# Kernel tuning notes

Measured on AMD Instinct MI355X. Metric: run time of the kernel, lower is better.

Reference implementation:

```python
import jax, jax.numpy as jnp
import numpy as np

B, S, V = 1, 4096, 50265
D, H, DH, FF, L = 768, 12, 64, 3072, 12
W = 256  # one-sided window (longformer-base attention_window=512)
EPS = 1e-5
NEG = -1e9


def _ln(x, s, b):
    mu = jnp.mean(x, -1, keepdims=True)
    var = jnp.mean(jnp.square(x - mu), -1, keepdims=True)
    return (x - mu) * jax.lax.rsqrt(var + EPS) * s + b


def _sliding_attn(q, k, v, key_mask):
    # q,k,v: [B,H,S,DH]; key_mask: [B,S] (1 = attend). Banded attention |i-j| <= W.
    b, h, s, dh = q.shape
    c = W
    nc = s // c
    idx = jnp.arange(nc)[:, None] * c + jnp.arange(3 * c)[None, :]  # index into padded key axis
    kp = jnp.pad(k, ((0, 0), (0, 0), (c, c), (0, 0)))
    vp = jnp.pad(v, ((0, 0), (0, 0), (c, c), (0, 0)))
    k3 = kp[:, :, idx]  # [B,H,nc,3c,DH]
    v3 = vp[:, :, idx]
    qc = q.reshape(b, h, nc, c, dh)
    scores = jnp.einsum('bhncd,bhnmd->bhncm', qc, k3) * (1.0 / (dh ** 0.5))
    rel = jnp.arange(3 * c)[None, :] - c - jnp.arange(c)[:, None]  # key_pos - query_pos, [c,3c]
    band = jnp.abs(rel) <= W
    km = jnp.pad(key_mask.astype(bool), ((0, 0), (c, c)))[:, idx]  # [B,nc,3c]
    valid = band[None, None, None] & km[:, None, :, None, :]
    probs = jax.nn.softmax(jnp.where(valid, scores, NEG), axis=-1)
    out = jnp.einsum('bhncm,bhnmd->bhncd', probs, v3)
    return out.reshape(b, h, s, dh)


def _forward(input_ids, attention_mask, word_emb, pos_emb, emb_ln_s, emb_ln_b,
             Wq, bq, Wk, bk, Wv, bv, Wo, bo, ln1_s, ln1_b,
             W1, b1, W2, b2, ln2_s, ln2_b,
             h1w, h1b, h2w, h2b, h3w, h3b):
    b, s = input_ids.shape
    pos = jnp.arange(s) + 2  # roberta-style position offset (padding_idx=1)
    x = word_emb[input_ids] + pos_emb[pos][None]
    x = _ln(x, emb_ln_s, emb_ln_b)
    key_mask = attention_mask

    def block(xc, p):
        wq, bq_, wk, bk_, wv, bv_, wo, bo_, l1s, l1b, w1, b1_, w2, b2_, l2s, l2b = p
        q = (xc @ wq + bq_).reshape(b, s, H, DH).transpose(0, 2, 1, 3)
        k = (xc @ wk + bk_).reshape(b, s, H, DH).transpose(0, 2, 1, 3)
        v = (xc @ wv + bv_).reshape(b, s, H, DH).transpose(0, 2, 1, 3)
        a = _sliding_attn(q, k, v, key_mask).transpose(0, 2, 1, 3).reshape(b, s, D)
        xc = _ln(xc + a @ wo + bo_, l1s, l1b)
        hdd = jax.nn.gelu(xc @ w1 + b1_, approximate=False)
        xc = _ln(xc + hdd @ w2 + b2_, l2s, l2b)
        return xc, None

    x, _ = jax.lax.scan(block, x, (Wq, bq, Wk, bk, Wv, bv, Wo, bo,
                                   ln1_s, ln1_b, W1, b1, W2, b2, ln2_s, ln2_b))

    # gather hidden state at last occurrence of token id 2 (</s>) per row
    eq = (input_ids == 2).astype(jnp.int32)
    sep = s - 1 - jnp.argmax(eq[:, ::-1], axis=1)
    emb = x[jnp.arange(b), sep]  # [B, D]

    z = jax.nn.relu(emb @ h1w + h1b)
    z = jax.nn.relu(z @ h2w + h2b)
    return jnp.tanh(z @ h3w + h3b)  # [B, 1]


def setup_inputs() -> dict:
    key = jax.random.key(0)
    ks = jax.random.split(key, 24)
    sc = 0.02

    def n(k, shape):
        return jax.random.normal(k, shape, jnp.float32) * sc

    input_ids = jax.random.randint(ks[0], (B, S), 0, V)
    input_ids = input_ids.at[:, -1].set(2)  # guarantee a </s> token (id 2)
    attention_mask = jnp.ones((B, S), jnp.int32)
    return {
        'input_ids': input_ids,
        'attention_mask': attention_mask,
        'word_emb': n(ks[1], (V, D)),
        'pos_emb': n(ks[2], (S + 2, D)),
        'emb_ln_s': jnp.ones((D,), jnp.float32),
        'emb_ln_b': jnp.zeros((D,), jnp.float32),
        'Wq': n(ks[3], (L, D, D)), 'bq': jnp.zeros((L, D), jnp.float32),
        'Wk': n(ks[4], (L, D, D)), 'bk': jnp.zeros((L, D), jnp.float32),
        'Wv': n(ks[5], (L, D, D)), 'bv': jnp.zeros((L, D), jnp.float32),
        'Wo': n(ks[6], (L, D, D)), 'bo': jnp.zeros((L, D), jnp.float32),
        'ln1_s': jnp.ones((L, D), jnp.float32), 'ln1_b': jnp.zeros((L, D), jnp.float32),
        'W1': n(ks[7], (L, D, FF)), 'b1': jnp.zeros((L, FF), jnp.float32),
        'W2': n(ks[8], (L, FF, D)), 'b2': jnp.zeros((L, D), jnp.float32),
        'ln2_s': jnp.ones((L, D), jnp.float32), 'ln2_b': jnp.zeros((L, D), jnp.float32),
        'h1w': n(ks[9], (D, 512)), 'h1b': jnp.zeros((512,), jnp.float32),
        'h2w': n(ks[10], (512, 256)), 'h2b': jnp.zeros((256,), jnp.float32),
        'h3w': n(ks[11], (256, 1)), 'h3b': jnp.zeros((1,), jnp.float32),
    }


def reference(input_ids, attention_mask, word_emb, pos_emb, emb_ln_s, emb_ln_b,
              Wq, bq, Wk, bk, Wv, bv, Wo, bo, ln1_s, ln1_b,
              W1, b1, W2, b2, ln2_s, ln2_b,
              h1w, h1b, h2w, h2b, h3w, h3b):
    return _forward(input_ids, attention_mask, word_emb, pos_emb, emb_ln_s, emb_ln_b,
                    Wq, bq, Wk, bk, Wv, bv, Wo, bo, ln1_s, ln1_b,
                    W1, b1, W2, b2, ln2_s, ln2_b,
                    h1w, h1b, h2w, h2b, h3w, h3b)
```

## Files before the change

kernel.cpp:

```cpp
#include <hip/hip_runtime.h>
#include <math.h>

#define S_LEN 4096
#define DMODEL 768
#define NHEAD 12
#define DHEAD 64
#define FFDIM 3072
#define NLAYER 12
#define WIN 256
#define QKVN 2304

typedef __bf16 bf16x8 __attribute__((ext_vector_type(8)));
typedef unsigned short u16x8 __attribute__((ext_vector_type(8)));
typedef float f32x4 __attribute__((ext_vector_type(4)));

__device__ inline unsigned short f2bf(float f) {
    unsigned int u = __float_as_uint(f);
    u += 0x7fff + ((u >> 16) & 1);
    return (unsigned short)(u >> 16);
}

__device__ inline void gload16(const void* g, void* l) {
    __builtin_amdgcn_global_load_lds((const __attribute__((address_space(1))) void*)g,
                                     (__attribute__((address_space(3))) void*)l, 16, 0, 0);
}


__device__ inline void block_reduce2(float& sum, float& sq) {
    #pragma unroll
    for (int off = 32; off; off >>= 1) {
        sum += __shfl_xor(sum, off);
        sq  += __shfl_xor(sq, off);
    }
    __shared__ float red[8];
    int wid = threadIdx.x >> 6, lane = threadIdx.x & 63;
    if (lane == 0) { red[wid] = sum; red[wid + 4] = sq; }
    __syncthreads();
    sum = red[0] + red[1] + red[2] + red[3];
    sq  = red[4] + red[5] + red[6] + red[7];
    __syncthreads();
}

__global__ __launch_bounds__(256) void ln_kernel(const float* __restrict__ in,
                                                 const float* __restrict__ s,
                                                 const float* __restrict__ b,
                                                 float* __restrict__ out,
                                                 unsigned short* __restrict__ outb) {
    int row = blockIdx.x, tid = threadIdx.x;
    const float* p = in + (size_t)row * DMODEL;
    float v0 = p[tid], v1 = p[tid + 256], v2 = p[tid + 512];
    float sum = v0 + v1 + v2;
    float sq  = v0 * v0 + v1 * v1 + v2 * v2;
    block_reduce2(sum, sq);
    float mu = sum * (1.0f / DMODEL);
    float var = sq * (1.0f / DMODEL) - mu * mu;
    float rs = rsqrtf(var + 1e-5f);
    float* o = out + (size_t)row * DMODEL;
    unsigned short* ob = outb + (size_t)row * DMODEL;
    float r0 = (v0 - mu) * rs * s[tid]       + b[tid];
    float r1 = (v1 - mu) * rs * s[tid + 256] + b[tid + 256];
    float r2 = (v2 - mu) * rs * s[tid + 512] + b[tid + 512];
    o[tid] = r0; o[tid + 256] = r1; o[tid + 512] = r2;
    ob[tid] = f2bf(r0); ob[tid + 256] = f2bf(r1); ob[tid + 512] = f2bf(r2);
}

__global__ __launch_bounds__(256) void embed_ln_kernel(const int* __restrict__ ids,
                                                       const float* __restrict__ wemb,
                                                       const float* __restrict__ pemb,
                                                       const float* __restrict__ s,
                                                       const float* __restrict__ b,
                                                       float* __restrict__ out,
                                                       unsigned short* __restrict__ outb) {
    int row = blockIdx.x, tid = threadIdx.x;
    int id = ids[row];
    const float* wp = wemb + (size_t)id * DMODEL;
    const float* pp = pemb + (size_t)(row + 2) * DMODEL;
    float v0 = wp[tid] + pp[tid];
    float v1 = wp[tid + 256] + pp[tid + 256];
    float v2 = wp[tid + 512] + pp[tid + 512];
    float sum = v0 + v1 + v2;
    float sq  = v0 * v0 + v1 * v1 + v2 * v2;
    block_reduce2(sum, sq);
    float mu = sum * (1.0f / DMODEL);
    float var = sq * (1.0f / DMODEL) - mu * mu;
    float rs = rsqrtf(var + 1e-5f);
    float* o = out + (size_t)row * DMODEL;
    unsigned short* ob = outb + (size_t)row * DMODEL;
    float r0 = (v0 - mu) * rs * s[tid]       + b[tid];
    float r1 = (v1 - mu) * rs * s[tid + 256] + b[tid + 256];
    float r2 = (v2 - mu) * rs * s[tid + 512] + b[tid + 512];
    o[tid] = r0; o[tid + 256] = r1; o[tid + 512] = r2;
    ob[tid] = f2bf(r0); ob[tid + 256] = f2bf(r1); ob[tid + 512] = f2bf(r2);
}

__global__ __launch_bounds__(256) void transpose_all(const float* __restrict__ wq,
                                                     const float* __restrict__ wk,
                                                     const float* __restrict__ wv,
                                                     const float* __restrict__ wo,
                                                     const float* __restrict__ w1,
                                                     const float* __restrict__ w2,
                                                     unsigned short* __restrict__ dq,
                                                     unsigned short* __restrict__ dk,
                                                     unsigned short* __restrict__ dv,
                                                     unsigned short* __restrict__ dwo,
                                                     unsigned short* __restrict__ d1,
                                                     unsigned short* __restrict__ d2) {
    const int id = blockIdx.x;
    const float* src; unsigned short* dst; int C, R, bx, by;
    if (id < 2304) {
        const int m = id / 576, t2 = id % 576;
        src = (m == 0) ? wq : (m == 1) ? wk : (m == 2) ? wv : wo;
        dst = (m == 0) ? dq : (m == 1) ? dk : (m == 2) ? dv : dwo;
        R = 768; C = 768; bx = (t2 % 24) * 32; by = (t2 / 24) * 32;
    } else if (id < 4608) {
        const int t2 = id - 2304;
        src = w1; dst = d1; R = 768; C = 3072;
        bx = (t2 % 96) * 32; by = (t2 / 96) * 32;
    } else {
        const int t2 = id - 4608;
        src = w2; dst = d2; R = 3072; C = 768;
        bx = (t2 % 24) * 32; by = (t2 / 24) * 32;
    }
    __shared__ float tile[32][33];
    const int t = threadIdx.x;
    const int lrow = t >> 3;
    const int lcol = (t & 7) * 4;
    float4 v = *(const float4*)&src[(size_t)(by + lrow) * C + bx + lcol];
    tile[lrow][lcol]     = v.x;
    tile[lrow][lcol + 1] = v.y;
    tile[lrow][lcol + 2] = v.z;
    tile[lrow][lcol + 3] = v.w;
    __syncthreads();
    const int c  = t >> 3;
    const int rp = t & 7;
    unsigned int b0 = f2bf(tile[4 * rp][c]);
    unsigned int b1 = f2bf(tile[4 * rp + 1][c]);
    unsigned int b2 = f2bf(tile[4 * rp + 2][c]);
    unsigned int b3 = f2bf(tile[4 * rp + 3][c]);
    uint2 pk;
    pk.x = (b1 << 16) | b0;
    pk.y = (b3 << 16) | b2;
    *(uint2*)&dst[(size_t)(bx + c) * R + by + 4 * rp] = pk;
}

__global__ __launch_bounds__(256) void bias_concat(const float* __restrict__ bq,
                                                   const float* __restrict__ bk,
                                                   const float* __restrict__ bv,
                                                   float* __restrict__ out) {
    int l = blockIdx.x, t = threadIdx.x;
    for (int i = t; i < DMODEL; i += 256) {
        out[(size_t)l * QKVN + i]              = bq[(size_t)l * DMODEL + i];
        out[(size_t)l * QKVN + DMODEL + i]     = bk[(size_t)l * DMODEL + i];
        out[(size_t)l * QKVN + 2 * DMODEL + i] = bv[(size_t)l * DMODEL + i];
    }
}

template<int MODE, int BN>
__global__ __launch_bounds__(256) void mfma_gemm(const unsigned short* __restrict__ A,
                                                 const unsigned short* __restrict__ Bt,
                                                 const float* __restrict__ bias,
                                                 const float* __restrict__ res,
                                                 void* __restrict__ Cout,
                                                 int M, int N, int K) {
    constexpr int MR = (BN == 128) ? 4 : 2;
    __shared__ unsigned short As[128 * 64];
    __shared__ unsigned short Bs[BN * 64];
    const int tid = threadIdx.x;
    const int wv = tid >> 6, lane = tid & 63;
    const int bm = blockIdx.x * 128, bn = blockIdx.y * BN;
    const int wr = (BN == 128) ? (wv >> 1) * 64 : wv * 32;
    const int wc = (BN == 128) ? (wv & 1) * 64 : 0;
    const int l15 = lane & 15, g = lane >> 4;

    f32x4 acc[MR][4];
    #pragma unroll
    for (int m = 0; m < MR; ++m)
        #pragma unroll
        for (int n = 0; n < 4; ++n)
            #pragma unroll
            for (int e = 0; e < 4; ++e) acc[m][n][e] = 0.f;

    const int srow = tid >> 3;
    const int scol = (tid & 7) * 8;

    for (int k0 = 0; k0 < K; k0 += 64) {
        __syncthreads();
        #pragma unroll
        for (int c = 0; c < 4; ++c)
            gload16(A + (size_t)(bm + c * 32 + srow) * K + k0 + scol,
                    (char*)As + c * 4096 + wv * 1024);
        #pragma unroll
        for (int c = 0; c < BN / 32; ++c)
            gload16(Bt + (size_t)(bn + c * 32 + srow) * K + k0 + scol,
                    (char*)Bs + c * 4096 + wv * 1024);
        __syncthreads();
        #pragma unroll
        for (int kk = 0; kk < 2; ++kk) {
            bf16x8 af[MR], bfr[4];
            #pragma unroll
            for (int m = 0; m < MR; ++m)
                af[m] = *(const bf16x8*)(As + (wr + m * 16 + l15) * 64 + kk * 32 + g * 8);
            #pragma unroll
            for (int n = 0; n < 4; ++n)
                bfr[n] = *(const bf16x8*)(Bs + (wc + n * 16 + l15) * 64 + kk * 32 + g * 8);
            #pragma unroll
            for (int m = 0; m < MR; ++m)
                #pragma unroll
                for (int n = 0; n < 4; ++n)
                    acc[m][n] = __builtin_amdgcn_mfma_f32_16x16x32_bf16(af[m], bfr[n], acc[m][n], 0, 0, 0);
        }
    }

    #pragma unroll
    for (int m = 0; m < MR; ++m) {
        const int row0 = bm + wr + m * 16 + g * 4;
        #pragma unroll
        for (int n = 0; n < 4; ++n) {
            const int col = bn + wc + n * 16 + l15;
            const float bb = bias[col];
            #pragma unroll
            for (int r = 0; r < 4; ++r) {
                float v = acc[m][n][r] + bb;
                if (MODE == 0) {
                    v += res[(size_t)(row0 + r) * N + col];
                    ((float*)Cout)[(size_t)(row0 + r) * N + col] = v;
                } else if (MODE == 1) {
                    ((unsigned short*)Cout)[(size_t)(row0 + r) * N + col] = f2bf(v);
                } else {
                    float gv = 0.5f * v * (1.0f + erff(v * 0.70710678118654752f));
                    ((unsigned short*)Cout)[(size_t)(row0 + r) * N + col] = f2bf(gv);
                }
            }
        }
    }
}

__global__ __launch_bounds__(256) void attn_mfma(const unsigned short* __restrict__ qkv,
                                                 const int* __restrict__ msk,
                                                 unsigned short* __restrict__ aout) {
    __shared__ unsigned short Ks[2][64 * 64];
    __shared__ unsigned short Vt[2][64 * 64];
    __shared__ unsigned short Ps[4][16 * 64];
    const int tid = threadIdx.x;
    const int wv = tid >> 6, lane = tid & 63;
    const int l15 = lane & 15, g = lane >> 4;
    const int h = blockIdx.y;
    const int q0 = blockIdx.x * 64;

    const int qrow = q0 + wv * 16 + l15;
    bf16x8 qf[2];
    #pragma unroll
    for (int kk = 0; kk < 2; ++kk)
        qf[kk] = *(const bf16x8*)(qkv + (size_t)qrow * QKVN + h * 64 + kk * 32 + g * 8);

    f32x4 o[4];
    #pragma unroll
    for (int n = 0; n < 4; ++n)
        #pragma unroll
        for (int e = 0; e < 4; ++e) o[n][e] = 0.f;
    float mst[4] = {-3e38f, -3e38f, -3e38f, -3e38f};
    float lst[4] = {0.f, 0.f, 0.f, 0.f};

    const int srow = tid >> 3;
    const int scol = (tid & 7) * 8;
    const int xr  = (l15 & 7) << 3;
    const int xb  = (scol >> 3) & 7;

    {
        const int kc = q0 - 256;
        #pragma unroll
        for (int cc = 0; cc < 2; ++cc) {
            const int r = cc * 32 + srow;
            int krow = min(max(kc + r, 0), S_LEN - 1);
            gload16(qkv + (size_t)krow * QKVN + DMODEL + h * 64 + (scol ^ ((r & 7) << 3)),
                    (char*)Ks[0] + cc * 4096 + wv * 1024);
        }
        #pragma unroll
        for (int cc = 0; cc < 2; ++cc) {
            const int r = cc * 32 + srow;
            int vrow = min(max(kc + r, 0), S_LEN - 1);
            u16x8 vvv = *(const u16x8*)(qkv + (size_t)vrow * QKVN + 2 * DMODEL + h * 64 + scol);
            #pragma unroll
            for (int j = 0; j < 8; ++j)
                Vt[0][(scol + j) * 64 + (r ^ ((xb ^ j) << 3))] = vvv[j];
        }
        __syncthreads();
    }

    for (int c = 0; c < 9; ++c) {
        const int cur = c & 1, nxt = cur ^ 1;
        const int kc = q0 - 256 + c * 64;

        if (c < 8) {
            const int kcn = kc + 64;
            #pragma unroll
            for (int cc = 0; cc < 2; ++cc) {
                const int r = cc * 32 + srow;
                int krow = min(max(kcn + r, 0), S_LEN - 1);
                gload16(qkv + (size_t)krow * QKVN + DMODEL + h * 64 + (scol ^ ((r & 7) << 3)),
                        (char*)Ks[nxt] + cc * 4096 + wv * 1024);
            }
            #pragma unroll
            for (int cc = 0; cc < 2; ++cc) {
                const int r = cc * 32 + srow;
                int vrow = min(max(kcn + r, 0), S_LEN - 1);
                u16x8 vvv = *(const u16x8*)(qkv + (size_t)vrow * QKVN + 2 * DMODEL + h * 64 + scol);
                #pragma unroll
                for (int j = 0; j < 8; ++j)
                    Vt[nxt][(scol + j) * 64 + (r ^ ((xb ^ j) << 3))] = vvv[j];
            }
        }

        f32x4 s[4];
        #pragma unroll
        for (int n = 0; n < 4; ++n)
            #pragma unroll
            for (int e = 0; e < 4; ++e) s[n][e] = 0.f;
        #pragma unroll
        for (int kk = 0; kk < 2; ++kk) {
            #pragma unroll
            for (int n = 0; n < 4; ++n) {
                bf16x8 kf = *(const bf16x8*)(Ks[cur] + (n * 16 + l15) * 64 + ((kk * 32 + g * 8) ^ xr));
                s[n] = __builtin_amdgcn_mfma_f32_16x16x32_bf16(qf[kk], kf, s[n], 0, 0, 0);
            }
        }

        float pv[4][4];
        const int qbase = q0 + wv * 16 + g * 4;
        #pragma unroll
        for (int n = 0; n < 4; ++n) {
            const int key = kc + n * 16 + l15;
            const bool kin = (key >= 0) && (key < S_LEN);
            const int mv = kin ? msk[key] : 0;
            #pragma unroll
            for (int r = 0; r < 4; ++r) {
                const int qa = qbase + r;
                const bool valid = (mv != 0) && (abs(key - qa) <= WIN);
                pv[n][r] = valid ? s[n][r] * 0.125f : -1e9f;
            }
        }
        float scold[4];
        #pragma unroll
        for (int r = 0; r < 4; ++r) {
            float mx = fmaxf(fmaxf(pv[0][r], pv[1][r]), fmaxf(pv[2][r], pv[3][r]));
            mx = fmaxf(mx, __shfl_xor(mx, 1));
            mx = fmaxf(mx, __shfl_xor(mx, 2));
            mx = fmaxf(mx, __shfl_xor(mx, 4));
            mx = fmaxf(mx, __shfl_xor(mx, 8));
            const float nm = fmaxf(mst[r], mx);
            scold[r] = expf(mst[r] - nm);
            float sum = 0.f;
            #pragma unroll
            for (int n = 0; n < 4; ++n) { pv[n][r] = expf(pv[n][r] - nm); sum += pv[n][r]; }
            sum += __shfl_xor(sum, 1); sum += __shfl_xor(sum, 2);
            sum += __shfl_xor(sum, 4); sum += __shfl_xor(sum, 8);
            lst[r] = lst[r] * scold[r] + sum;
            mst[r] = nm;
        }
        #pragma unroll
        for (int n = 0; n < 4; ++n)
            #pragma unroll
            for (int r = 0; r < 4; ++r)
                o[n][r] *= scold[r];

        #pragma unroll
        for (int n = 0; n < 4; ++n)
            #pragma unroll
            for (int r = 0; r < 4; ++r) {
                const int ql = g * 4 + r;
                Ps[wv][ql * 64 + ((n * 16 + l15) ^ ((ql & 7) << 3))] = f2bf(pv[n][r]);
            }

        #pragma unroll
        for (int kk = 0; kk < 2; ++kk) {
            bf16x8 pf = *(const bf16x8*)(Ps[wv] + l15 * 64 + ((kk * 32 + g * 8) ^ xr));
            #pragma unroll
            for (int nd = 0; nd < 4; ++nd) {
                const int d = nd * 16 + l15;
                const int xv = (((nd * 2 + (l15 >> 3)) & 7) ^ (l15 & 7)) << 3;
                bf16x8 vf = *(const bf16x8*)(Vt[cur] + d * 64 + ((kk * 32 + g * 8) ^ xv));
                o[nd] = __builtin_amdgcn_mfma_f32_16x16x32_bf16(pf, vf, o[nd], 0, 0, 0);
            }
        }

        __syncthreads();
    }

    #pragma unroll
    for (int r = 0; r < 4; ++r) {
        const float inv = 1.0f / lst[r];
        const int qa = q0 + wv * 16 + g * 4 + r;
        #pragma unroll
        for (int nd = 0; nd < 4; ++nd)
            aout[(size_t)qa * DMODEL + h * 64 + nd * 16 + l15] = f2bf(o[nd][r] * inv);
    }
}

__global__ __launch_bounds__(256) void head1_kernel(const int* __restrict__ ids,
                                                    const float* __restrict__ x,
                                                    const float* __restrict__ w1,
                                                    const float* __restrict__ b1,
                                                    float* __restrict__ z1) {
    const int tid = threadIdx.x;
    __shared__ int sred[256];
    int loc = -1;
    for (int i = tid; i < S_LEN; i += 256)
        if (ids[i] == 2) loc = i;
    sred[tid] = loc;
    __syncthreads();
    for (int s2 = 128; s2; s2 >>= 1) {
        if (tid < s2) sred[tid] = max(sred[tid], sred[tid + s2]);
        __syncthreads();
    }
    const int sep = sred[0] < 0 ? (S_LEN - 1) : sred[0];

    __shared__ float emb[DMODEL];
    for (int d = tid; d < DMODEL; d += 256) emb[d] = x[(size_t)sep * DMODEL + d];
    __syncthreads();

    const int o = blockIdx.x * 64 + (tid & 63);
    const int chunk = tid >> 6;
    float s = 0.f;
    const int d0 = chunk * 192;
    for (int d = d0; d < d0 + 192; ++d)
        s += emb[d] * w1[(size_t)d * 512 + o];
    __shared__ float part[4][64];
    part[chunk][tid & 63] = s;
    __syncthreads();
    if (chunk == 0) {
        float v = part[0][tid] + part[1][tid] + part[2][tid] + part[3][tid] + b1[o];
        z1[o] = fmaxf(v, 0.f);
    }
}

__global__ __launch_bounds__(256) void head2_kernel(const float* __restrict__ z1,
                                                    const float* __restrict__ w2,
                                                    const float* __restrict__ b2,
                                                    const float* __restrict__ w3,
                                                    const float* __restrict__ b3,
                                                    float* __restrict__ out) {
    const int tid = threadIdx.x;
    __shared__ float z1s[512];
    for (int i = tid; i < 512; i += 256) z1s[i] = z1[i];
    __syncthreads();
    float s = b2[tid];
    for (int d = 0; d < 512; ++d) s += z1s[d] * w2[(size_t)d * 256 + tid];
    float z2 = fmaxf(s, 0.f);
    __shared__ float fred[256];
    fred[tid] = z2 * w3[tid];
    __syncthreads();
    for (int s2 = 128; s2; s2 >>= 1) {
        if (tid < s2) fred[tid] += fred[tid + s2];
        __syncthreads();
    }
    if (tid == 0) out[0] = tanhf(fred[0] + b3[0]);
}


extern "C" void kernel_launch(void* const* d_in, const int* in_sizes, int n_in,
                              void* d_out, int out_size, void* d_ws, size_t ws_size,
                              hipStream_t stream) {
    const int*   ids      = (const int*)d_in[0];
    const int*   amask    = (const int*)d_in[1];
    const float* word_emb = (const float*)d_in[2];
    const float* pos_emb  = (const float*)d_in[3];
    const float* emb_s    = (const float*)d_in[4];
    const float* emb_b    = (const float*)d_in[5];
    const float* Wq = (const float*)d_in[6];
    const float* bq = (const float*)d_in[7];
    const float* Wk = (const float*)d_in[8];
    const float* bk = (const float*)d_in[9];
    const float* Wv = (const float*)d_in[10];
    const float* bv = (const float*)d_in[11];
    const float* Wo = (const float*)d_in[12];
    const float* bo = (const float*)d_in[13];
    const float* l1s = (const float*)d_in[14];
    const float* l1b = (const float*)d_in[15];
    const float* W1 = (const float*)d_in[16];
    const float* b1 = (const float*)d_in[17];
    const float* W2 = (const float*)d_in[18];
    const float* b2 = (const float*)d_in[19];
    const float* l2s = (const float*)d_in[20];
    const float* l2b = (const float*)d_in[21];
    const float* h1w = (const float*)d_in[22];
    const float* h1b = (const float*)d_in[23];
    const float* h2w = (const float*)d_in[24];
    const float* h2b = (const float*)d_in[25];
    const float* h3w = (const float*)d_in[26];
    const float* h3b = (const float*)d_in[27];

    char* ws = (char*)d_ws;
    float* x          = (float*)(ws);
    float* t          = (float*)(ws + 12582912);
    unsigned short* xb   = (unsigned short*)(ws + 25165824);
    unsigned short* qkv  = (unsigned short*)(ws + 31457280);
    unsigned short* a    = (unsigned short*)(ws + 50331648);
    unsigned short* hb   = (unsigned short*)(ws + 56623104);
    unsigned short* WqkvT= (unsigned short*)(ws + 81788928);
    unsigned short* WoT  = (unsigned short*)(ws + 85327872);
    unsigned short* W1T  = (unsigned short*)(ws + 86507520);
    unsigned short* W2T  = (unsigned short*)(ws + 91226112);
    float* biascat       = (float*)(ws + 95944704);
    float* z1ws          = (float*)(ws + 96055296);

    bias_concat<<<NLAYER, 256, 0, stream>>>(bq, bk, bv, biascat);
    embed_ln_kernel<<<S_LEN, 256, 0, stream>>>(ids, word_emb, pos_emb, emb_s, emb_b, x, xb);

    const size_t dd = (size_t)DMODEL * DMODEL;
    const size_t df = (size_t)DMODEL * FFDIM;

    for (int l = 0; l < NLAYER; ++l) {
        transpose_all<<<6912, 256, 0, stream>>>(Wq + l * dd, Wk + l * dd, Wv + l * dd, Wo + l * dd,
                                                W1 + l * df, W2 + l * df,
                                                WqkvT, WqkvT + dd, WqkvT + 2 * dd, WoT, W1T, W2T);

        mfma_gemm<1, 128><<<dim3(32, 18), 256, 0, stream>>>(xb, WqkvT, biascat + (size_t)l * QKVN,
                                                            nullptr, qkv, S_LEN, QKVN, DMODEL);
        attn_mfma<<<dim3(S_LEN / 64, NHEAD), 256, 0, stream>>>(qkv, amask, a);

        mfma_gemm<0, 64><<<dim3(32, 12), 256, 0, stream>>>(a, WoT, bo + (size_t)l * DMODEL,
                                                           x, t, S_LEN, DMODEL, DMODEL);
        ln_kernel<<<S_LEN, 256, 0, stream>>>(t, l1s + (size_t)l * DMODEL, l1b + (size_t)l * DMODEL, x, xb);

        mfma_gemm<2, 128><<<dim3(32, 24), 256, 0, stream>>>(xb, W1T, b1 + (size_t)l * FFDIM,
                                                            nullptr, hb, S_LEN, FFDIM, DMODEL);
        mfma_gemm<0, 64><<<dim3(32, 12), 256, 0, stream>>>(hb, W2T, b2 + (size_t)l * DMODEL,
                                                           x, t, S_LEN, DMODEL, FFDIM);
        ln_kernel<<<S_LEN, 256, 0, stream>>>(t, l2s + (size_t)l * DMODEL, l2b + (size_t)l * DMODEL, x, xb);
    }

    head1_kernel<<<8, 256, 0, stream>>>(ids, x, h1w, h1b, z1ws);
    head2_kernel<<<1, 256, 0, stream>>>(z1ws, h2w, h2b, h3w, h3b, (float*)d_out);
}
```

Baseline: 2.774 ms.

## Use one wave per row in LayerNorm and single-buffer attention K/V with vectorized V transpose

The LayerNorm kernel now handles four rows per block, one wavefront per row, with float4 loads and stores and a pure shuffle reduction, so the shared-memory reduction and block barriers go away. The attention kernel drops K/V double buffering in favour of a single LDS buffer loaded each chunk. The V transpose now gathers 4x4 tiles with 8-byte loads and writes 4-element vectors into LDS instead of scalar 16-bit stores. This lowers LDS use and store instruction count, but loses the overlap of the next chunk's loads with the current chunk's MFMA work.

```diff
diff --git a/kernel.cpp b/kernel.cpp
--- a/kernel.cpp
+++ b/kernel.cpp
@@ -12,6 +12,7 @@
 
 typedef __bf16 bf16x8 __attribute__((ext_vector_type(8)));
 typedef unsigned short u16x8 __attribute__((ext_vector_type(8)));
+typedef unsigned short u16x4 __attribute__((ext_vector_type(4)));
 typedef float f32x4 __attribute__((ext_vector_type(4)));
 
 __device__ inline unsigned short f2bf(float f) {
@@ -23,22 +24,6 @@
 __device__ inline void gload16(const void* g, void* l) {
     __builtin_amdgcn_global_load_lds((const __attribute__((address_space(1))) void*)g,
                                      (__attribute__((address_space(3))) void*)l, 16, 0, 0);
-}
-
-
-__device__ inline void block_reduce2(float& sum, float& sq) {
-    #pragma unroll
-    for (int off = 32; off; off >>= 1) {
-        sum += __shfl_xor(sum, off);
-        sq  += __shfl_xor(sq, off);
-    }
-    __shared__ float red[8];
-    int wid = threadIdx.x >> 6, lane = threadIdx.x & 63;
-    if (lane == 0) { red[wid] = sum; red[wid + 4] = sq; }
-    __syncthreads();
-    sum = red[0] + red[1] + red[2] + red[3];
-    sq  = red[4] + red[5] + red[6] + red[7];
-    __syncthreads();
 }
 
 __global__ __launch_bounds__(256) void ln_kernel(const float* __restrict__ in,
@@ -46,22 +31,59 @@
                                                  const float* __restrict__ b,
                                                  float* __restrict__ out,
                                                  unsigned short* __restrict__ outb) {
-    int row = blockIdx.x, tid = threadIdx.x;
+    const int wv = threadIdx.x >> 6, lane = threadIdx.x & 63;
+    const int row = blockIdx.x * 4 + wv;
     const float* p = in + (size_t)row * DMODEL;
-    float v0 = p[tid], v1 = p[tid + 256], v2 = p[tid + 512];
-    float sum = v0 + v1 + v2;
-    float sq  = v0 * v0 + v1 * v1 + v2 * v2;
-    block_reduce2(sum, sq);
-    float mu = sum * (1.0f / DMODEL);
-    float var = sq * (1.0f / DMODEL) - mu * mu;
-    float rs = rsqrtf(var + 1e-5f);
+    const int c = lane * 4;
+    float4 v0 = *(const float4*)&p[c];
+    float4 v1 = *(const float4*)&p[c + 256];
+    float4 v2 = *(const float4*)&p[c + 512];
+    float sum = v0.x + v0.y + v0.z + v0.w + v1.x + v1.y + v1.z + v1.w
+              + v2.x + v2.y + v2.z + v2.w;
+    float sq  = v0.x*v0.x + v0.y*v0.y + v0.z*v0.z + v0.w*v0.w
+              + v1.x*v1.x + v1.y*v1.y + v1.z*v1.z + v1.w*v1.w
+              + v2.x*v2.x + v2.y*v2.y + v2.z*v2.z + v2.w*v2.w;
+    #pragma unroll
+    for (int off = 32; off; off >>= 1) {
+        sum += __shfl_xor(sum, off);
+        sq  += __shfl_xor(sq, off);
+    }
+    const float mu = sum * (1.0f / DMODEL);
+    const float var = sq * (1.0f / DMODEL) - mu * mu;
+    const float rs = rsqrtf(var + 1e-5f);
     float* o = out + (size_t)row * DMODEL;
     unsigned short* ob = outb + (size_t)row * DMODEL;
-    float r0 = (v0 - mu) * rs * s[tid]       + b[tid];
-    float r1 = (v1 - mu) * rs * s[tid + 256] + b[tid + 256];
-    float r2 = (v2 - mu) * rs * s[tid + 512] + b[tid + 512];
-    o[tid] = r0; o[tid + 256] = r1; o[tid + 512] = r2;
-    ob[tid] = f2bf(r0); ob[tid + 256] = f2bf(r1); ob[tid + 512] = f2bf(r2);
+    #pragma unroll
+    for (int seg = 0; seg < 3; ++seg) {
+        const int cc = c + seg * 256;
+        float4 v = (seg == 0) ? v0 : (seg == 1) ? v1 : v2;
+        float4 sv = *(const float4*)&s[cc];
+        float4 bv = *(const float4*)&b[cc];
+        float4 r;
+        r.x = (v.x - mu) * rs * sv.x + bv.x;
+        r.y = (v.y - mu) * rs * sv.y + bv.y;
+        r.z = (v.z - mu) * rs * sv.z + bv.z;
+        r.w = (v.w - mu) * rs * sv.w + bv.w;
+        *(float4*)&o[cc] = r;
+        u16x4 pk;
+        pk[0] = f2bf(r.x); pk[1] = f2bf(r.y); pk[2] = f2bf(r.z); pk[3] = f2bf(r.w);
+        *(u16x4*)&ob[cc] = pk;
+    }
+}
+
+__device__ inline void block_reduce2(float& sum, float& sq) {
+    #pragma unroll
+    for (int off = 32; off; off >>= 1) {
+        sum += __shfl_xor(sum, off);
+        sq  += __shfl_xor(sq, off);
+    }
+    __shared__ float red[8];
+    int wid = threadIdx.x >> 6, lane = threadIdx.x & 63;
+    if (lane == 0) { red[wid] = sum; red[wid + 4] = sq; }
+    __syncthreads();
+    sum = red[0] + red[1] + red[2] + red[3];
+    sq  = red[4] + red[5] + red[6] + red[7];
+    __syncthreads();
 }
 
 __global__ __launch_bounds__(256) void embed_ln_kernel(const int* __restrict__ ids,
@@ -238,8 +260,8 @@
 __global__ __launch_bounds__(256) void attn_mfma(const unsigned short* __restrict__ qkv,
                                                  const int* __restrict__ msk,
                                                  unsigned short* __restrict__ aout) {
-    __shared__ unsigned short Ks[2][64 * 64];
-    __shared__ unsigned short Vt[2][64 * 64];
+    __shared__ unsigned short Ks[64 * 64];
+    __shared__ unsigned short Vt[64 * 64];
     __shared__ unsigned short Ps[4][16 * 64];
     const int tid = threadIdx.x;
     const int wv = tid >> 6, lane = tid & 63;
@@ -264,52 +286,36 @@
     const int srow = tid >> 3;
     const int scol = (tid & 7) * 8;
     const int xr  = (l15 & 7) << 3;
-    const int xb  = (scol >> 3) & 7;
-
-    {
-        const int kc = q0 - 256;
+    const int kg4 = (tid >> 4) * 4;
+    const int dg4 = (tid & 15) * 4;
+
+    for (int c = 0; c < 9; ++c) {
+        const int kc = q0 - 256 + c * 64;
+        __syncthreads();
         #pragma unroll
         for (int cc = 0; cc < 2; ++cc) {
             const int r = cc * 32 + srow;
             int krow = min(max(kc + r, 0), S_LEN - 1);
             gload16(qkv + (size_t)krow * QKVN + DMODEL + h * 64 + (scol ^ ((r & 7) << 3)),
-                    (char*)Ks[0] + cc * 4096 + wv * 1024);
-        }
-        #pragma unroll
-        for (int cc = 0; cc < 2; ++cc) {
-            const int r = cc * 32 + srow;
-            int vrow = min(max(kc + r, 0), S_LEN - 1);
-            u16x8 vvv = *(const u16x8*)(qkv + (size_t)vrow * QKVN + 2 * DMODEL + h * 64 + scol);
-            #pragma unroll
-            for (int j = 0; j < 8; ++j)
-                Vt[0][(scol + j) * 64 + (r ^ ((xb ^ j) << 3))] = vvv[j];
+                    (char*)Ks + cc * 4096 + wv * 1024);
+        }
+        {
+            u16x4 vr[4];
+            #pragma unroll
+            for (int j = 0; j < 4; ++j) {
+                int vrow = min(max(kc + kg4 + j, 0), S_LEN - 1);
+                vr[j] = *(const u16x4*)(qkv + (size_t)vrow * QKVN + 2 * DMODEL + h * 64 + dg4);
+            }
+            #pragma unroll
+            for (int i = 0; i < 4; ++i) {
+                const int d = dg4 + i;
+                const int f = ((d >> 3) ^ d) & 7;
+                u16x4 w;
+                w[0] = vr[0][i]; w[1] = vr[1][i]; w[2] = vr[2][i]; w[3] = vr[3][i];
+                *(u16x4*)(Vt + d * 64 + (kg4 ^ (f << 3))) = w;
+            }
         }
         __syncthreads();
-    }
-
-    for (int c = 0; c < 9; ++c) {
-        const int cur = c & 1, nxt = cur ^ 1;
-        const int kc = q0 - 256 + c * 64;
-
-        if (c < 8) {
-            const int kcn = kc + 64;
-            #pragma unroll
-            for (int cc = 0; cc < 2; ++cc) {
-                const int r = cc * 32 + srow;
-                int krow = min(max(kcn + r, 0), S_LEN - 1);
-                gload16(qkv + (size_t)krow * QKVN + DMODEL + h * 64 + (scol ^ ((r & 7) << 3)),
-                        (char*)Ks[nxt] + cc * 4096 + wv * 1024);
-            }
-            #pragma unroll
-            for (int cc = 0; cc < 2; ++cc) {
-                const int r = cc * 32 + srow;
-                int vrow = min(max(kcn + r, 0), S_LEN - 1);
-                u16x8 vvv = *(const u16x8*)(qkv + (size_t)vrow * QKVN + 2 * DMODEL + h * 64 + scol);
-                #pragma unroll
-                for (int j = 0; j < 8; ++j)
-                    Vt[nxt][(scol + j) * 64 + (r ^ ((xb ^ j) << 3))] = vvv[j];
-            }
-        }
 
         f32x4 s[4];
         #pragma unroll
@@ -320,7 +326,7 @@
         for (int kk = 0; kk < 2; ++kk) {
             #pragma unroll
             for (int n = 0; n < 4; ++n) {
-                bf16x8 kf = *(const bf16x8*)(Ks[cur] + (n * 16 + l15) * 64 + ((kk * 32 + g * 8) ^ xr));
+                bf16x8 kf = *(const bf16x8*)(Ks + (n * 16 + l15) * 64 + ((kk * 32 + g * 8) ^ xr));
                 s[n] = __builtin_amdgcn_mfma_f32_16x16x32_bf16(qf[kk], kf, s[n], 0, 0, 0);
             }
         }
@@ -378,12 +384,10 @@
             for (int nd = 0; nd < 4; ++nd) {
                 const int d = nd * 16 + l15;
                 const int xv = (((nd * 2 + (l15 >> 3)) & 7) ^ (l15 & 7)) << 3;
-                bf16x8 vf = *(const bf16x8*)(Vt[cur] + d * 64 + ((kk * 32 + g * 8) ^ xv));
+                bf16x8 vf = *(const bf16x8*)(Vt + d * 64 + ((kk * 32 + g * 8) ^ xv));
                 o[nd] = __builtin_amdgcn_mfma_f32_16x16x32_bf16(pf, vf, o[nd], 0, 0, 0);
             }
         }
-
-        __syncthreads();
     }
 
     #pragma unroll
@@ -520,13 +524,13 @@
 
         mfma_gemm<0, 64><<<dim3(32, 12), 256, 0, stream>>>(a, WoT, bo + (size_t)l * DMODEL,
                                                            x, t, S_LEN, DMODEL, DMODEL);
-        ln_kernel<<<S_LEN, 256, 0, stream>>>(t, l1s + (size_t)l * DMODEL, l1b + (size_t)l * DMODEL, x, xb);
+        ln_kernel<<<S_LEN / 4, 256, 0, stream>>>(t, l1s + (size_t)l * DMODEL, l1b + (size_t)l * DMODEL, x, xb);
 
         mfma_gemm<2, 128><<<dim3(32, 24), 256, 0, stream>>>(xb, W1T, b1 + (size_t)l * FFDIM,
                                                             nullptr, hb, S_LEN, FFDIM, DMODEL);
         mfma_gemm<0, 64><<<dim3(32, 12), 256, 0, stream>>>(hb, W2T, b2 + (size_t)l * DMODEL,
                                                            x, t, S_LEN, DMODEL, FFDIM);
-        ln_kernel<<<S_LEN, 256, 0, stream>>>(t, l2s + (size_t)l * DMODEL, l2b + (size_t)l * DMODEL, x, xb);
+        ln_kernel<<<S_LEN / 4, 256, 0, stream>>>(t, l2s + (size_t)l * DMODEL, l2b + (size_t)l * DMODEL, x, xb);
     }
 
     head1_kernel<<<8, 256, 0, stream>>>(ids, x, h1w, h1b, z1ws);
```

Result: no change. 2.755 ms (-0.7%).
